# Performance work log

Measured on AMD Instinct MI355X. Metric: run time of the kernel, lower is better.

## Reference

```python
import jax, jax.numpy as jnp
import numpy as np

B, C, H, W = 8, 128, 64, 64


def setup_inputs() -> dict:
    key = jax.random.key(0)
    ks = jax.random.split(key, 9)
    d = C
    return {
        "x": jax.random.normal(ks[0], (B, C, H, W), dtype=jnp.float32),
        "qw": jax.random.normal(ks[1], (d, d), dtype=jnp.float32),
        "qb": jax.random.normal(ks[2], (d,), dtype=jnp.float32),
        "kw": jax.random.normal(ks[3], (d, d), dtype=jnp.float32),
        "kb": jax.random.normal(ks[4], (d,), dtype=jnp.float32),
        "vw": jax.random.normal(ks[5], (d, d), dtype=jnp.float32),
        "vb": jax.random.normal(ks[6], (d,), dtype=jnp.float32),
        "proj_w": jax.random.normal(ks[7], (d, d), dtype=jnp.float32),
        "proj_b": jax.random.normal(ks[8], (d,), dtype=jnp.float32),
    }


def reference(x, qw, qb, kw, kb, vw, vb, proj_w, proj_b):
    b, c, h, w = x.shape
    n = h * w  # number of spatial tokens
    # permute to channels-last and flatten spatial dims: (b, n, c)
    xt = jnp.transpose(x, (0, 2, 3, 1)).reshape(b, n, c)
    q = xt @ qw + qb
    k = xt @ kw + kb
    v = xt @ vw + vb
    scale = c ** (-0.5)
    # full (n x n) attention over flattened spatial tokens, single head
    attn = jax.nn.softmax(jnp.einsum("bnc,bmc->bnm", q, k) * scale, axis=-1)
    hout = jnp.einsum("bnm,bmc->bnc", attn, v) @ proj_w + proj_b
    out = xt + hout  # residual is on the permuted (channels-last) x, per source
    return out.reshape(b, h, w, c)
```

## Files before the change

### kernel.cpp

```cpp
#include <hip/hip_runtime.h>

#define NB 8
#define CD 128
#define NN 4096
#define SCALE 0.08838834764831845f
#define L2E 1.44269504088896f

typedef __bf16 bf16x8 __attribute__((ext_vector_type(8)));
typedef float f32x4 __attribute__((ext_vector_type(4)));

__device__ __forceinline__ unsigned swz256(unsigned row, unsigned b) {
  unsigned s = b >> 4, o = b & 15u;
  unsigned sw = (s & 8u) | ((s & 7u) ^ (row & 7u));
  return row * 256u + sw * 16u + o;
}
__device__ __forceinline__ unsigned swz128(unsigned row, unsigned b) {
  unsigned s = b >> 4, o = b & 15u;
  unsigned sw = (s ^ row) & 7u;
  return row * 128u + sw * 16u + o;
}

__global__ __launch_bounds__(256, 2) void qkv_kernel(
    const float* __restrict__ x,
    const float* __restrict__ qw, const float* __restrict__ qb,
    const float* __restrict__ kw, const float* __restrict__ kb,
    const float* __restrict__ vw, const float* __restrict__ vb,
    __bf16* __restrict__ Qh, __bf16* __restrict__ Ql,
    __bf16* __restrict__ Kh, __bf16* __restrict__ Kl,
    __bf16* __restrict__ Vt)
{
  __shared__ __align__(16) unsigned char sm[49664];
  const int tid = threadIdx.x;
  const int lane = tid & 63, wv = tid >> 6;
  const int l15 = lane & 15, g = lane >> 4;
  const int b = blockIdx.y;
  const int n0 = blockIdx.x * 64;
  const f32x4 Z4 = {0.f, 0.f, 0.f, 0.f};

  #pragma unroll 4
  for (int i = 0; i < 32; ++i) {
    int e = i * 256 + tid;
    int nl = e & 63, c = e >> 6;
    float f = x[((size_t)(b * CD + c)) * NN + n0 + nl];
    __bf16 h = (__bf16)f;
    __bf16 lo = (__bf16)(f - (float)h);
    unsigned off = swz256((unsigned)nl, (unsigned)(c * 2));
    *(__bf16*)(sm + off) = h;
    *(__bf16*)(sm + 16384 + off) = lo;
  }
  __syncthreads();

  bf16x8 ah[4], al[4];
  #pragma unroll
  for (int kk = 0; kk < 4; ++kk) {
    unsigned off = swz256((unsigned)(wv * 16 + l15), (unsigned)(kk * 64 + g * 16));
    ah[kk] = *(const bf16x8*)(sm + off);
    al[kk] = *(const bf16x8*)(sm + 16384 + off);
  }

  for (int mat = 0; mat < 2; ++mat) {
    const float* gw = mat ? kw : qw;
    const float* gb = mat ? kb : qb;
    __bf16* Oh = mat ? Kh : Qh;
    __bf16* Ol = mat ? Kl : Ql;
    const float sc = mat ? 1.0f : SCALE;
    for (int qd = 0; qd < 4; ++qd) {
      #pragma unroll 4
      for (int i = 0; i < 16; ++i) {
        int e = i * 256 + tid;
        int dl = e & 31, c = e >> 5;
        float f = gw[c * CD + qd * 32 + dl];
        __bf16 h = (__bf16)f;
        __bf16 lo = (__bf16)(f - (float)h);
        unsigned off = swz256((unsigned)dl, (unsigned)(c * 2));
        *(__bf16*)(sm + 32768 + off) = h;
        *(__bf16*)(sm + 40960 + off) = lo;
      }
      __syncthreads();
      #pragma unroll
      for (int fr = 0; fr < 2; ++fr) {
        f32x4 acc = Z4;
        #pragma unroll
        for (int kk = 0; kk < 4; ++kk) {
          unsigned off = swz256((unsigned)(fr * 16 + l15), (unsigned)(kk * 64 + g * 16));
          bf16x8 bh = *(const bf16x8*)(sm + 32768 + off);
          bf16x8 bl = *(const bf16x8*)(sm + 40960 + off);
          acc = __builtin_amdgcn_mfma_f32_16x16x32_bf16(ah[kk], bh, acc, 0, 0, 0);
          acc = __builtin_amdgcn_mfma_f32_16x16x32_bf16(ah[kk], bl, acc, 0, 0, 0);
          acc = __builtin_amdgcn_mfma_f32_16x16x32_bf16(al[kk], bh, acc, 0, 0, 0);
        }
        const int dout = qd * 32 + fr * 16 + l15;
        const float bias = gb[dout];
        #pragma unroll
        for (int r = 0; r < 4; ++r) {
          int row = n0 + wv * 16 + g * 4 + r;
          float v = (acc[r] + bias) * sc;
          __bf16 h = (__bf16)v;
          __bf16 lo = (__bf16)(v - (float)h);
          size_t go = ((size_t)(b * NN + row)) * CD + dout;
          Oh[go] = h;
          Ol[go] = lo;
        }
      }
      __syncthreads();
    }
  }

  f32x4 accV[8];
  #pragma unroll
  for (int i = 0; i < 8; ++i) accV[i] = Z4;
  for (int qd = 0; qd < 4; ++qd) {
    #pragma unroll 4
    for (int i = 0; i < 16; ++i) {
      int e = i * 256 + tid;
      int dl = e & 31, c = e >> 5;
      float f = vw[c * CD + qd * 32 + dl];
      *(__bf16*)(sm + 32768 + swz256((unsigned)dl, (unsigned)(c * 2))) = (__bf16)f;
    }
    __syncthreads();
    #pragma unroll
    for (int fr = 0; fr < 2; ++fr) {
      f32x4 acc = accV[qd * 2 + fr];
      #pragma unroll
      for (int kk = 0; kk < 4; ++kk) {
        unsigned off = swz256((unsigned)(fr * 16 + l15), (unsigned)(kk * 64 + g * 16));
        bf16x8 bh = *(const bf16x8*)(sm + 32768 + off);
        acc = __builtin_amdgcn_mfma_f32_16x16x32_bf16(ah[kk], bh, acc, 0, 0, 0);
      }
      accV[qd * 2 + fr] = acc;
    }
    __syncthreads();
  }
  #pragma unroll
  for (int df = 0; df < 8; ++df) {
    int dout = df * 16 + l15;
    float bias = vb[dout];
    #pragma unroll
    for (int r = 0; r < 4; ++r) {
      int row = wv * 16 + g * 4 + r;
      *(__bf16*)(sm + 32768 + (row * 132 + dout) * 2) = (__bf16)(accV[df][r] + bias);
    }
  }
  __syncthreads();
  #pragma unroll 4
  for (int i = 0; i < 32; ++i) {
    int e = i * 256 + tid;
    int nl = e & 63, dout = e >> 6;
    __bf16 v = *(const __bf16*)(sm + 32768 + (nl * 132 + dout) * 2);
    Vt[((size_t)(b * CD + dout)) * NN + n0 + nl] = v;
  }
}

__global__ __launch_bounds__(256, 2) void attn_kernel(
    const __bf16* __restrict__ Qh, const __bf16* __restrict__ Ql,
    const __bf16* __restrict__ Kh, const __bf16* __restrict__ Kl,
    const __bf16* __restrict__ Vt, const float* __restrict__ x,
    const float* __restrict__ pw, const float* __restrict__ pb,
    float* __restrict__ out)
{
  __shared__ __align__(16) unsigned char sm[57344];
  const int tid = threadIdx.x;
  const int lane = tid & 63, wv = tid >> 6;
  const int l15 = lane & 15, g = lane >> 4;
  const int b = blockIdx.y;
  const int q0 = blockIdx.x * 64;
  const f32x4 Z4 = {0.f, 0.f, 0.f, 0.f};

  bf16x8 qh[4], ql[4];
  #pragma unroll
  for (int kk = 0; kk < 4; ++kk) {
    size_t off = ((size_t)(b * NN + q0 + wv * 16 + l15)) * CD + kk * 32 + g * 8;
    qh[kk] = *(const bf16x8*)(Qh + off);
    ql[kk] = *(const bf16x8*)(Ql + off);
  }

  f32x4 accO[8];
  #pragma unroll
  for (int i = 0; i < 8; ++i) accO[i] = Z4;
  float mrow[4], lrow[4];
  #pragma unroll
  for (int r = 0; r < 4; ++r) { mrow[r] = -__builtin_inff(); lrow[r] = 0.f; }

  bf16x8 pkh[4], pkl[4], pvv[4];
  const int rK = tid >> 4, sK = tid & 15;
  const int rV = tid >> 3, sV = tid & 7;

  #define ISSUE_TILE(KT)                                                        \
    {                                                                           \
      const size_t kb_ = (size_t)(b * NN + (KT) * 64);                          \
      _Pragma("unroll")                                                         \
      for (int i = 0; i < 4; ++i) {                                             \
        pkh[i] = *(const bf16x8*)(Kh + (kb_ + i * 16 + rK) * CD + sK * 8);      \
        pkl[i] = *(const bf16x8*)(Kl + (kb_ + i * 16 + rK) * CD + sK * 8);      \
        pvv[i] = *(const bf16x8*)(Vt + ((size_t)(b * CD) + i * 32 + rV) * NN +  \
                                  (KT) * 64 + sV * 8);                          \
      }                                                                         \
    }
  #define COMMIT_TILE()                                                         \
    {                                                                           \
      _Pragma("unroll")                                                         \
      for (int i = 0; i < 4; ++i) {                                             \
        unsigned o_ = swz256((unsigned)(i * 16 + rK), (unsigned)(sK * 16));     \
        *(bf16x8*)(sm + o_) = pkh[i];                                           \
        *(bf16x8*)(sm + 16384 + o_) = pkl[i];                                   \
        *(bf16x8*)(sm + 32768 +                                                 \
                   swz128((unsigned)(i * 32 + rV), (unsigned)(sV * 16))) = pvv[i]; \
      }                                                                         \
    }

  ISSUE_TILE(0);
  COMMIT_TILE();
  __syncthreads();

  for (int kt = 0; kt < 64; ++kt) {
    if (kt < 63) ISSUE_TILE(kt + 1);

    f32x4 s4[4];
    #pragma unroll
    for (int kf = 0; kf < 4; ++kf) s4[kf] = Z4;
    __builtin_amdgcn_s_setprio(1);
    #pragma unroll
    for (int kf = 0; kf < 4; ++kf) {
      #pragma unroll
      for (int kk = 0; kk < 4; ++kk) {
        unsigned off = swz256((unsigned)(kf * 16 + l15), (unsigned)(kk * 64 + g * 16));
        bf16x8 bh = *(const bf16x8*)(sm + off);
        bf16x8 bl = *(const bf16x8*)(sm + 16384 + off);
        s4[kf] = __builtin_amdgcn_mfma_f32_16x16x32_bf16(qh[kk], bh, s4[kf], 0, 0, 0);
        s4[kf] = __builtin_amdgcn_mfma_f32_16x16x32_bf16(qh[kk], bl, s4[kf], 0, 0, 0);
        s4[kf] = __builtin_amdgcn_mfma_f32_16x16x32_bf16(ql[kk], bh, s4[kf], 0, 0, 0);
      }
    }
    __builtin_amdgcn_s_setprio(0);

    float ps[4], mnew[4];
    bool grow = false;
    #pragma unroll
    for (int r = 0; r < 4; ++r) {
      float mx = fmaxf(fmaxf(s4[0][r], s4[1][r]), fmaxf(s4[2][r], s4[3][r]));
      mx = fmaxf(mx, __shfl_xor(mx, 1));
      mx = fmaxf(mx, __shfl_xor(mx, 2));
      mx = fmaxf(mx, __shfl_xor(mx, 4));
      mx = fmaxf(mx, __shfl_xor(mx, 8));
      float mn = fmaxf(mrow[r], mx);
      mnew[r] = mn;
      grow = grow || (mn > mrow[r]);
      float p0 = 0.f;
      #pragma unroll
      for (int kf = 0; kf < 4; ++kf) {
        float p = exp2f((s4[kf][r] - mn) * L2E);
        s4[kf][r] = p;
        p0 += p;
      }
      p0 += __shfl_xor(p0, 1);
      p0 += __shfl_xor(p0, 2);
      p0 += __shfl_xor(p0, 4);
      p0 += __shfl_xor(p0, 8);
      ps[r] = p0;
    }
    if (__any((int)grow)) {
      #pragma unroll
      for (int r = 0; r < 4; ++r) {
        float alpha = exp2f((mrow[r] - mnew[r]) * L2E);
        lrow[r] *= alpha;
        #pragma unroll
        for (int df = 0; df < 8; ++df) accO[df][r] *= alpha;
      }
    }
    #pragma unroll
    for (int r = 0; r < 4; ++r) { mrow[r] = mnew[r]; lrow[r] += ps[r]; }

    #pragma unroll
    for (int kf = 0; kf < 4; ++kf) {
      #pragma unroll
      for (int r = 0; r < 4; ++r) {
        unsigned row = (unsigned)(wv * 16 + g * 4 + r);
        *(__bf16*)(sm + 49152 + swz128(row, (unsigned)((kf * 16 + l15) * 2))) =
            (__bf16)s4[kf][r];
      }
    }

    bf16x8 pa[2];
    #pragma unroll
    for (int kk2 = 0; kk2 < 2; ++kk2)
      pa[kk2] = *(const bf16x8*)(sm + 49152 +
                  swz128((unsigned)(wv * 16 + l15), (unsigned)(kk2 * 64 + g * 16)));
    __builtin_amdgcn_s_setprio(1);
    #pragma unroll
    for (int df = 0; df < 8; ++df) {
      #pragma unroll
      for (int kk2 = 0; kk2 < 2; ++kk2) {
        bf16x8 bv = *(const bf16x8*)(sm + 32768 +
                      swz128((unsigned)(df * 16 + l15), (unsigned)(kk2 * 64 + g * 16)));
        accO[df] = __builtin_amdgcn_mfma_f32_16x16x32_bf16(pa[kk2], bv, accO[df], 0, 0, 0);
      }
    }
    __builtin_amdgcn_s_setprio(0);

    __syncthreads();
    if (kt < 63) COMMIT_TILE();
    __syncthreads();
  }
  #undef ISSUE_TILE
  #undef COMMIT_TILE

  float rl[4];
  #pragma unroll
  for (int r = 0; r < 4; ++r) rl[r] = 1.0f / lrow[r];
  #pragma unroll
  for (int df = 0; df < 8; ++df) {
    #pragma unroll
    for (int r = 0; r < 4; ++r) {
      unsigned row = (unsigned)(wv * 16 + g * 4 + r);
      *(__bf16*)(sm + swz256(row, (unsigned)((df * 16 + l15) * 2))) =
          (__bf16)(accO[df][r] * rl[r]);
    }
  }
  #pragma unroll 4
  for (int i = 0; i < 16; ++i) {
    int e = i * 256 + tid;
    int c = e >> 5, d4 = e & 31;
    const float4 w4 = *(const float4*)(pw + c * CD + d4 * 4);
    *(__bf16*)(sm + 16384 + swz256((unsigned)(d4 * 4 + 0), (unsigned)(c * 2))) = (__bf16)w4.x;
    *(__bf16*)(sm + 16384 + swz256((unsigned)(d4 * 4 + 1), (unsigned)(c * 2))) = (__bf16)w4.y;
    *(__bf16*)(sm + 16384 + swz256((unsigned)(d4 * 4 + 2), (unsigned)(c * 2))) = (__bf16)w4.z;
    *(__bf16*)(sm + 16384 + swz256((unsigned)(d4 * 4 + 3), (unsigned)(c * 2))) = (__bf16)w4.w;
  }
  __syncthreads();

  bf16x8 oa[4];
  #pragma unroll
  for (int kk = 0; kk < 4; ++kk)
    oa[kk] = *(const bf16x8*)(sm + swz256((unsigned)(wv * 16 + l15),
                                          (unsigned)(kk * 64 + g * 16)));
  #pragma unroll
  for (int df = 0; df < 8; ++df) {
    f32x4 acc = Z4;
    #pragma unroll
    for (int kk = 0; kk < 4; ++kk) {
      bf16x8 bw = *(const bf16x8*)(sm + 16384 +
                    swz256((unsigned)(df * 16 + l15), (unsigned)(kk * 64 + g * 16)));
      acc = __builtin_amdgcn_mfma_f32_16x16x32_bf16(oa[kk], bw, acc, 0, 0, 0);
    }
    const int cc = df * 16 + l15;
    const float bias = pb[cc];
    #pragma unroll
    for (int r = 0; r < 4; ++r) {
      int row = q0 + wv * 16 + g * 4 + r;
      float val = acc[r] + bias + x[((size_t)(b * CD + cc)) * NN + row];
      out[((size_t)(b * NN + row)) * CD + cc] = val;
    }
  }
}

extern "C" void kernel_launch(void* const* d_in, const int* in_sizes, int n_in,
                              void* d_out, int out_size, void* d_ws, size_t ws_size,
                              hipStream_t stream) {
  (void)in_sizes; (void)n_in; (void)out_size; (void)ws_size;
  const float* x  = (const float*)d_in[0];
  const float* qw = (const float*)d_in[1];
  const float* qb = (const float*)d_in[2];
  const float* kw = (const float*)d_in[3];
  const float* kb = (const float*)d_in[4];
  const float* vw = (const float*)d_in[5];
  const float* vb = (const float*)d_in[6];
  const float* pw = (const float*)d_in[7];
  const float* pb = (const float*)d_in[8];
  float* out = (float*)d_out;

  const size_t SZ = (size_t)NB * NN * CD;
  __bf16* Qh = (__bf16*)d_ws;
  __bf16* Ql = Qh + SZ;
  __bf16* Kh = Ql + SZ;
  __bf16* Kl = Kh + SZ;
  __bf16* Vt = Kl + SZ;

  dim3 grid(NN / 64, NB), blk(256);
  qkv_kernel<<<grid, blk, 0, stream>>>(x, qw, qb, kw, kb, vw, vb,
                                       Qh, Ql, Kh, Kl, Vt);
  attn_kernel<<<grid, blk, 0, stream>>>(Qh, Ql, Kh, Kl, Vt, x, pw, pb, out);
}
```

Baseline: 344.6 us.

## Fold log2e into Q scale, compute row sums via MFMA, DPP row-max reductions

Multiplies log2(e) into the Q scale so the softmax exp2 no longer needs a per-element multiply. The row-sum reduction moves from shuffles to an extra MFMA against a ones vector, and the row-max uses DPP row rotates instead of ds_swizzle shuffles. It also changes the P-tile LDS swizzle to reduce bank conflicts, linearizes the grid with batch innermost so concurrent blocks span different batches, and adds a sched_barrier after the prefetch. The trade-off is two extra MFMAs per tile, and the row sum is now taken from bf16-rounded P, which slightly changes numerics.

```diff
diff --git a/kernel.cpp b/kernel.cpp
--- a/kernel.cpp
+++ b/kernel.cpp
@@ -5,6 +5,7 @@
 #define NN 4096
 #define SCALE 0.08838834764831845f
 #define L2E 1.44269504088896f
+#define QSCALE (SCALE * L2E)
 
 typedef __bf16 bf16x8 __attribute__((ext_vector_type(8)));
 typedef float f32x4 __attribute__((ext_vector_type(4)));
@@ -19,6 +20,16 @@
   unsigned sw = (s ^ row) & 7u;
   return row * 128u + sw * 16u + o;
 }
+__device__ __forceinline__ unsigned swzP(unsigned row, unsigned b) {
+  unsigned s = b >> 4, o = b & 15u;
+  unsigned sw = (s ^ (row ^ (row >> 2))) & 7u;
+  return row * 128u + sw * 16u + o;
+}
+
+#define DPP_ROR_F(x, N)                                                       \
+  __builtin_bit_cast(float, __builtin_amdgcn_update_dpp(                      \
+      __builtin_bit_cast(int, (x)), __builtin_bit_cast(int, (x)),             \
+      0x120 + (N), 0xF, 0xF, false))
 
 __global__ __launch_bounds__(256, 2) void qkv_kernel(
     const float* __restrict__ x,
@@ -33,8 +44,8 @@
   const int tid = threadIdx.x;
   const int lane = tid & 63, wv = tid >> 6;
   const int l15 = lane & 15, g = lane >> 4;
-  const int b = blockIdx.y;
-  const int n0 = blockIdx.x * 64;
+  const int b = blockIdx.x & 7;
+  const int n0 = (blockIdx.x >> 3) * 64;
   const f32x4 Z4 = {0.f, 0.f, 0.f, 0.f};
 
   #pragma unroll 4
@@ -63,7 +74,7 @@
     const float* gb = mat ? kb : qb;
     __bf16* Oh = mat ? Kh : Qh;
     __bf16* Ol = mat ? Kl : Ql;
-    const float sc = mat ? 1.0f : SCALE;
+    const float sc = mat ? 1.0f : QSCALE;
     for (int qd = 0; qd < 4; ++qd) {
       #pragma unroll 4
       for (int i = 0; i < 16; ++i) {
@@ -162,8 +173,8 @@
   const int tid = threadIdx.x;
   const int lane = tid & 63, wv = tid >> 6;
   const int l15 = lane & 15, g = lane >> 4;
-  const int b = blockIdx.y;
-  const int q0 = blockIdx.x * 64;
+  const int b = blockIdx.x & 7;
+  const int q0 = (blockIdx.x >> 3) * 64;
   const f32x4 Z4 = {0.f, 0.f, 0.f, 0.f};
 
   bf16x8 qh[4], ql[4];
@@ -174,12 +185,20 @@
     ql[kk] = *(const bf16x8*)(Ql + off);
   }
 
+  bf16x8 bones;
+  {
+    __bf16 v = (l15 == 0) ? (__bf16)1.0f : (__bf16)0.0f;
+    #pragma unroll
+    for (int j = 0; j < 8; ++j) bones[j] = v;
+  }
+
   f32x4 accO[8];
   #pragma unroll
   for (int i = 0; i < 8; ++i) accO[i] = Z4;
-  float mrow[4], lrow[4];
-  #pragma unroll
-  for (int r = 0; r < 4; ++r) { mrow[r] = -__builtin_inff(); lrow[r] = 0.f; }
+  f32x4 accL = Z4;
+  float mrow[4];
+  #pragma unroll
+  for (int r = 0; r < 4; ++r) mrow[r] = -__builtin_inff();
 
   bf16x8 pkh[4], pkl[4], pvv[4];
   const int rK = tid >> 4, sK = tid & 15;
@@ -214,6 +233,7 @@
 
   for (int kt = 0; kt < 64; ++kt) {
     if (kt < 63) ISSUE_TILE(kt + 1);
+    __builtin_amdgcn_sched_barrier(0);
 
     f32x4 s4[4];
     #pragma unroll
@@ -233,49 +253,40 @@
     }
     __builtin_amdgcn_s_setprio(0);
 
-    float ps[4], mnew[4];
+    float mnew[4];
     bool grow = false;
     #pragma unroll
     for (int r = 0; r < 4; ++r) {
       float mx = fmaxf(fmaxf(s4[0][r], s4[1][r]), fmaxf(s4[2][r], s4[3][r]));
-      mx = fmaxf(mx, __shfl_xor(mx, 1));
-      mx = fmaxf(mx, __shfl_xor(mx, 2));
-      mx = fmaxf(mx, __shfl_xor(mx, 4));
-      mx = fmaxf(mx, __shfl_xor(mx, 8));
+      mx = fmaxf(mx, DPP_ROR_F(mx, 8));
+      mx = fmaxf(mx, DPP_ROR_F(mx, 4));
+      mx = fmaxf(mx, DPP_ROR_F(mx, 2));
+      mx = fmaxf(mx, DPP_ROR_F(mx, 1));
       float mn = fmaxf(mrow[r], mx);
       mnew[r] = mn;
       grow = grow || (mn > mrow[r]);
-      float p0 = 0.f;
-      #pragma unroll
-      for (int kf = 0; kf < 4; ++kf) {
-        float p = exp2f((s4[kf][r] - mn) * L2E);
-        s4[kf][r] = p;
-        p0 += p;
-      }
-      p0 += __shfl_xor(p0, 1);
-      p0 += __shfl_xor(p0, 2);
-      p0 += __shfl_xor(p0, 4);
-      p0 += __shfl_xor(p0, 8);
-      ps[r] = p0;
+      #pragma unroll
+      for (int kf = 0; kf < 4; ++kf)
+        s4[kf][r] = exp2f(s4[kf][r] - mn);
     }
     if (__any((int)grow)) {
       #pragma unroll
       for (int r = 0; r < 4; ++r) {
-        float alpha = exp2f((mrow[r] - mnew[r]) * L2E);
-        lrow[r] *= alpha;
+        float alpha = exp2f(mrow[r] - mnew[r]);
+        accL[r] *= alpha;
         #pragma unroll
         for (int df = 0; df < 8; ++df) accO[df][r] *= alpha;
       }
     }
     #pragma unroll
-    for (int r = 0; r < 4; ++r) { mrow[r] = mnew[r]; lrow[r] += ps[r]; }
+    for (int r = 0; r < 4; ++r) mrow[r] = mnew[r];
 
     #pragma unroll
     for (int kf = 0; kf < 4; ++kf) {
       #pragma unroll
       for (int r = 0; r < 4; ++r) {
         unsigned row = (unsigned)(wv * 16 + g * 4 + r);
-        *(__bf16*)(sm + 49152 + swz128(row, (unsigned)((kf * 16 + l15) * 2))) =
+        *(__bf16*)(sm + 49152 + swzP(row, (unsigned)((kf * 16 + l15) * 2))) =
             (__bf16)s4[kf][r];
       }
     }
@@ -284,8 +295,10 @@
     #pragma unroll
     for (int kk2 = 0; kk2 < 2; ++kk2)
       pa[kk2] = *(const bf16x8*)(sm + 49152 +
-                  swz128((unsigned)(wv * 16 + l15), (unsigned)(kk2 * 64 + g * 16)));
+                  swzP((unsigned)(wv * 16 + l15), (unsigned)(kk2 * 64 + g * 16)));
     __builtin_amdgcn_s_setprio(1);
+    accL = __builtin_amdgcn_mfma_f32_16x16x32_bf16(pa[0], bones, accL, 0, 0, 0);
+    accL = __builtin_amdgcn_mfma_f32_16x16x32_bf16(pa[1], bones, accL, 0, 0, 0);
     #pragma unroll
     for (int df = 0; df < 8; ++df) {
       #pragma unroll
@@ -306,7 +319,10 @@
 
   float rl[4];
   #pragma unroll
-  for (int r = 0; r < 4; ++r) rl[r] = 1.0f / lrow[r];
+  for (int r = 0; r < 4; ++r) {
+    float lv = __shfl(accL[r], lane & 48);
+    rl[r] = 1.0f / lv;
+  }
   #pragma unroll
   for (int df = 0; df < 8; ++df) {
     #pragma unroll
@@ -375,7 +391,7 @@
   __bf16* Kl = Kh + SZ;
   __bf16* Vt = Kl + SZ;
 
-  dim3 grid(NN / 64, NB), blk(256);
+  dim3 grid(512), blk(256);
   qkv_kernel<<<grid, blk, 0, stream>>>(x, qw, qb, kw, kb, vw, vb,
                                        Qh, Ql, Kh, Kl, Vt);
   attn_kernel<<<grid, blk, 0, stream>>>(Qh, Ql, Kh, Kl, Vt, x, pw, pb, out);
```

New measurement: 300.4 us. 12.8% less time.
